# Performance work log

Measured on AMD Instinct MI355X. Metric: run time of the kernel, lower is better.

Reference implementation:

```python
import jax, jax.numpy as jnp
import numpy as np

# Mamba2 config (from AdapterMamba: d_model=1024, n_layer=4, headdim=32; mamba_ssm defaults)
D_MODEL = 1024
N_LAYER = 4
EXPAND = 2
HEADDIM = 32
D_STATE = 128
D_CONV = 4
NGROUPS = 1
D_INNER = EXPAND * D_MODEL            # 2048
NHEADS = D_INNER // HEADDIM           # 64
CONV_DIM = D_INNER + 2 * NGROUPS * D_STATE   # 2304
D_IN_PROJ = 2 * D_INNER + 2 * NGROUPS * D_STATE + NHEADS  # 4416
BATCH, SEQLEN = 4, 2048


def setup_inputs() -> dict:
    key = jax.random.key(0)
    ks = jax.random.split(key, 8)
    x = jax.random.normal(ks[0], (BATCH, SEQLEN, D_MODEL), jnp.float32)
    s_in = 1.0 / np.sqrt(D_MODEL)
    s_out = 1.0 / np.sqrt(D_INNER)
    W_in = jax.random.normal(ks[1], (N_LAYER, D_MODEL, D_IN_PROJ), jnp.float32) * s_in
    conv_w = jax.random.normal(ks[2], (N_LAYER, CONV_DIM, D_CONV), jnp.float32) * 0.5
    conv_b = jnp.zeros((N_LAYER, CONV_DIM), jnp.float32)
    # dt_bias = softplus^{-1}(dt) for dt in [1e-3, 0.1] (mamba dt_init)
    dt = jax.random.uniform(ks[3], (N_LAYER, NHEADS), jnp.float32, 0.001, 0.1)
    dt_bias = jnp.log(jnp.expm1(dt))
    # A in [1, 16] per head (A_init_range)
    A_log = jnp.log(jax.random.uniform(ks[4], (N_LAYER, NHEADS), jnp.float32, 1.0, 16.0))
    D = jnp.ones((N_LAYER, NHEADS), jnp.float32)
    gate_norm_w = jnp.ones((N_LAYER, D_INNER), jnp.float32)
    W_out = jax.random.normal(ks[5], (N_LAYER, D_INNER, D_MODEL), jnp.float32) * s_out
    block_norm_w = jnp.ones((N_LAYER, D_MODEL), jnp.float32)
    final_norm_w = jnp.ones((D_MODEL,), jnp.float32)
    return dict(x=x, W_in=W_in, conv_w=conv_w, conv_b=conv_b, dt_bias=dt_bias,
                A_log=A_log, D=D, gate_norm_w=gate_norm_w, W_out=W_out,
                block_norm_w=block_norm_w, final_norm_w=final_norm_w)


def _rmsnorm(x, w, eps=1e-5):
    return x * jax.lax.rsqrt(jnp.mean(x * x, axis=-1, keepdims=True) + eps) * w


def _mamba2_layer(h, Wi, cw, cb, dtb, Alog, Dh, gw, Wo):
    B, L, _ = h.shape
    zxbcdt = h @ Wi                                        # [B,L,4416]
    z, xBC, dt = jnp.split(zxbcdt, [D_INNER, D_INNER + CONV_DIM], axis=-1)
    # causal depthwise conv1d, width D_CONV, over (x, B, C) channels
    xp = jnp.pad(xBC, ((0, 0), (D_CONV - 1, 0), (0, 0)))
    conv = cb + sum(xp[:, k:k + L, :] * cw[:, k] for k in range(D_CONV))
    xBC = jax.nn.silu(conv)
    xs, Bm, Cm = jnp.split(xBC, [D_INNER, D_INNER + D_STATE], axis=-1)
    xs = xs.reshape(B, L, NHEADS, HEADDIM)                 # [B,L,H,P]
    dt = jax.nn.softplus(dt + dtb)                         # [B,L,H]
    A = -jnp.exp(Alog)                                     # [H]
    dA = jnp.exp(dt * A)                                   # [B,L,H]
    dtx = dt[..., None] * xs                               # [B,L,H,P]

    def step(hs, inp):
        dA_t, dtx_t, B_t, C_t = inp
        # hs: [B,H,P,N]
        hs = hs * dA_t[:, :, None, None] + dtx_t[..., None] * B_t[:, None, None, :]
        y = jnp.einsum('bhpn,bn->bhp', hs, C_t)
        return hs, y

    h0 = jnp.zeros((B, NHEADS, HEADDIM, D_STATE), h.dtype)
    _, ys = jax.lax.scan(step, h0, (dA.swapaxes(0, 1), dtx.swapaxes(0, 1),
                                    Bm.swapaxes(0, 1), Cm.swapaxes(0, 1)))
    y = ys.swapaxes(0, 1) + Dh[None, None, :, None] * xs   # skip term D*x
    y = y.reshape(B, L, D_INNER)
    y = _rmsnorm(y * jax.nn.silu(z), gw)                   # gated RMSNorm (Mamba2)
    return y @ Wo


def reference(x, W_in, conv_w, conv_b, dt_bias, A_log, D, gate_norm_w, W_out,
              block_norm_w, final_norm_w):
    h = x
    for l in range(N_LAYER):
        h = h + _mamba2_layer(_rmsnorm(h, block_norm_w[l]), W_in[l], conv_w[l],
                              conv_b[l], dt_bias[l], A_log[l], D[l],
                              gate_norm_w[l], W_out[l])
    return _rmsnorm(h, final_norm_w)
```

## Files before the change

kernel.cpp:

```cpp
#include <hip/hip_runtime.h>

typedef unsigned short u16;
typedef __bf16 bf16x8 __attribute__((ext_vector_type(8)));
typedef float f32x4 __attribute__((ext_vector_type(4)));
typedef u16 u16x8 __attribute__((ext_vector_type(8)));

#define NLAYER 4
#define DMODEL 1024
#define DINNER 2048
#define NHEADS 64
#define CONVDIM 2304
#define XBCLD 2368
#define DPROJ 4416
#define DPROJP 4608
#define BATCH 4
#define SEQLEN 2048
#define NTOK 8192
#define QC 64
#define NCH (SEQLEN / QC)

__device__ __forceinline__ u16 f2bf(float f) {
  union { float f; unsigned u; } v; v.f = f;
  return (u16)((v.u + 0x7fffu + ((v.u >> 16) & 1u)) >> 16);
}
__device__ __forceinline__ float bf2f(u16 h) {
  union { unsigned u; float f; } v; v.u = (unsigned)h << 16; return v.f;
}

__device__ __forceinline__ float block_sum256(float v) {
  __shared__ float red[4];
  #pragma unroll
  for (int o = 32; o; o >>= 1) v += __shfl_xor(v, o);
  int t = threadIdx.x;
  if ((t & 63) == 0) red[t >> 6] = v;
  __syncthreads();
  return red[0] + red[1] + red[2] + red[3];
}

__device__ __forceinline__ int swz128(int row, int g) { return (row << 7) + (((g ^ (row & 7)) << 3)); }
__device__ __forceinline__ int swz64(int row, int g)  { return (row << 6) + (((g ^ (row & 7)) << 3)); }

#define GLDS16(g, s) __builtin_amdgcn_global_load_lds( \
    (const __attribute__((address_space(1))) void*)(g), \
    (__attribute__((address_space(3))) void*)(s), 16, 0, 0)

#define PH_READ(buf, p)                                                        \
  if ((p) == 0) {                                                              \
    _Pragma("unroll") for (int nf = 0; nf < NF; ++nf)                          \
    _Pragma("unroll") for (int ks = 0; ks < 2; ++ks)                           \
      breg[nf][ks] = readB(buf, nf, ks);                                       \
  }                                                                            \
  _Pragma("unroll") for (int i = 0; i < 2; ++i)                                \
  _Pragma("unroll") for (int ks = 0; ks < 2; ++ks)                             \
    ar[i][ks] = readA(buf, ((p) << 1) + i, ks);

#define PH_TAIL(buf, p)                                                        \
  __builtin_amdgcn_sched_barrier(0);                                           \
  __builtin_amdgcn_s_barrier();                                                \
  asm volatile("s_waitcnt lgkmcnt(0)" ::: "memory");                           \
  __builtin_amdgcn_sched_barrier(0);                                           \
  __builtin_amdgcn_s_setprio(1);                                               \
  _Pragma("unroll") for (int i = 0; i < 2; ++i)                                \
  _Pragma("unroll") for (int nf = 0; nf < NF; ++nf)                            \
  _Pragma("unroll") for (int ks = 0; ks < 2; ++ks)                             \
    acc[((p) << 1) + i][nf] = __builtin_amdgcn_mfma_f32_16x16x32_bf16(         \
        ar[i][ks], breg[nf][ks], acc[((p) << 1) + i][nf], 0, 0, 0);            \
  __builtin_amdgcn_s_setprio(0);                                               \
  __builtin_amdgcn_s_barrier();

template<int NF, int MODE>
__global__ __launch_bounds__(512, 1) void gemm8p_k(
    const u16* __restrict__ A, const u16* __restrict__ Bt,
    float* __restrict__ C, u16* __restrict__ zy, u16* __restrict__ xbc,
    float* __restrict__ dtraw, int K, int nt2) {
  constexpr int NBH = NF / 2;
  __shared__ __align__(16) u16 smem[(2 * (2 + NBH)) * 8192];

  const int tid = threadIdx.x;
  const int w = tid >> 6, l = tid & 63;
  const int wm = w >> 2, wn = w & 3;
  const int l16 = l & 15, kg = l >> 4;
  const int lr = l >> 3, lc = l & 7;
  const int swg = lc ^ lr;

  const int gx = gridDim.x;
  const int nwg = gx * gridDim.y;
  int bid = blockIdx.y * gx + blockIdx.x;
  bid = (bid & 7) * (nwg >> 3) + (bid >> 3);
  const int m0 = (bid / gx) << 8;
  const int n0 = (bid % gx) * (NF << 6);

  f32x4 acc[8][NF] = {};
  bf16x8 breg[NF][2];
  bf16x8 ar[2][2];

  auto stageA = [&](int buf, int h, int kt) {
    const size_t kb = (size_t)(kt << 6) + (swg << 3);
    u16* dst = smem + (((buf << 1) + h) << 13);
    #pragma unroll
    for (int j = 0; j < 2; ++j)
      GLDS16(A + (size_t)(m0 + (h << 7) + (j << 6) + (w << 3) + lr) * K + kb,
             dst + (j << 12) + (w << 9));
  };
  auto stageB = [&](int buf, int h, int kt) {
    const size_t kb = (size_t)(kt << 6) + (swg << 3);
    u16* dst = smem + ((4 + buf * NBH + h) << 13);
    #pragma unroll
    for (int j = 0; j < 2; ++j)
      GLDS16(Bt + (size_t)(n0 + (h << 7) + (j << 6) + (w << 3) + lr) * K + kb,
             dst + (j << 12) + (w << 9));
  };
  auto readA = [&](int buf, int mf, int ks) -> bf16x8 {
    const int r = (mf << 4) + l16;
    return *(const bf16x8*)&smem[(((buf << 1) + wm) << 13) + (r << 6) + ((((ks << 2) + kg) ^ (r & 7)) << 3)];
  };
  auto readB = [&](int buf, int nf, int ks) -> bf16x8 {
    const int row = wn * (NF << 4) + (nf << 4) + l16;
    const int bh = row >> 7, r = row & 127;
    return *(const bf16x8*)&smem[((4 + buf * NBH + bh) << 13) + (r << 6) + ((((ks << 2) + kg) ^ (r & 7)) << 3)];
  };

  stageA(0, 0, 0); stageA(0, 1, 0);
  #pragma unroll
  for (int h = 0; h < NBH; ++h) stageB(0, h, 0);
  #pragma unroll
  for (int h = 0; h < NBH; ++h) stageB(1, h, 1);
  asm volatile("s_waitcnt vmcnt(%0) lgkmcnt(0)" :: "n"(2 * NBH) : "memory");
  __builtin_amdgcn_sched_barrier(0);
  __builtin_amdgcn_s_barrier();

  for (int t = 0; t < nt2; ++t) {
    const int kt0 = t << 1;
    const bool more = (t + 1 < nt2);
    PH_READ(0, 0)
    stageA(1, 0, kt0 + 1);
    PH_TAIL(0, 0)
    PH_READ(0, 1)
    stageA(1, 1, kt0 + 1);
    PH_TAIL(0, 1)
    PH_READ(0, 2)
    if (more) stageB(0, 0, kt0 + 2);
    PH_TAIL(0, 2)
    PH_READ(0, 3)
    if (more && NBH == 2) stageB(0, 1, kt0 + 2);
    if (more) { asm volatile("s_waitcnt vmcnt(%0)" :: "n"(2 * NBH) : "memory"); }
    else      { asm volatile("s_waitcnt vmcnt(0)" ::: "memory"); }
    PH_TAIL(0, 3)
    PH_READ(1, 0)
    if (more) stageA(0, 0, kt0 + 2);
    PH_TAIL(1, 0)
    PH_READ(1, 1)
    if (more) stageA(0, 1, kt0 + 2);
    PH_TAIL(1, 1)
    PH_READ(1, 2)
    if (more) stageB(1, 0, kt0 + 3);
    PH_TAIL(1, 2)
    PH_READ(1, 3)
    if (more && NBH == 2) stageB(1, 1, kt0 + 3);
    if (more) { asm volatile("s_waitcnt vmcnt(%0)" :: "n"(2 * NBH) : "memory"); }
    PH_TAIL(1, 3)
  }

  __syncthreads();
  if (MODE == 1) {
    const int nt = n0 >> 8;
    if (nt == 17) {
      if (wn == 0) {
        #pragma unroll
        for (int mf = 0; mf < 8; ++mf) {
          const int row = m0 + (wm << 7) + (mf << 4) + (kg << 2);
          #pragma unroll
          for (int nf = 0; nf < NF; ++nf) {
            const int dc = (nf << 4) + l16;
            #pragma unroll
            for (int r = 0; r < 4; ++r)
              dtraw[(size_t)(row + r) * 64 + dc] = acc[mf][nf][r];
          }
        }
      }
    } else {
      #pragma unroll
      for (int mf = 0; mf < 8; ++mf) {
        #pragma unroll
        for (int nf = 0; nf < NF; ++nf) {
          const int col = (wn << 6) + (nf << 4) + l16;
          #pragma unroll
          for (int r = 0; r < 4; ++r) {
            const int row = (wm << 7) + (mf << 4) + (kg << 2) + r;
            smem[(row << 8) + (((col >> 3) ^ (row & 7)) << 3) + (col & 7)] = f2bf(acc[mf][nf][r]);
          }
        }
      }
      __syncthreads();
      const int g = l & 31;
      #pragma unroll
      for (int j = 0; j < 16; ++j) {
        const int row = (w << 5) + (j << 1) + (l >> 5);
        u16x8 v = *(const u16x8*)&smem[(row << 8) + ((g ^ (row & 7)) << 3)];
        const size_t grow = (size_t)(m0 + row);
        const int gcol = n0 + (g << 3);
        if (nt < 8) *(u16x8*)&zy[grow * DINNER + gcol] = v;
        else        *(u16x8*)&xbc[grow * XBCLD + (gcol - 2048)] = v;
      }
    }
  } else {
    float* smf = (float*)smem;
    #pragma unroll
    for (int pass = 0; pass < 2; ++pass) {
      if (wm == pass) {
        #pragma unroll
        for (int mf = 0; mf < 8; ++mf) {
          #pragma unroll
          for (int nf = 0; nf < NF; ++nf) {
            const int col = (wn << 5) + (nf << 4) + l16;
            #pragma unroll
            for (int r = 0; r < 4; ++r) {
              const int lrow = (mf << 4) + (kg << 2) + r;
              smf[(lrow << 7) + (((col >> 2) ^ (lrow & 7)) << 2) + (col & 3)] = acc[mf][nf][r];
            }
          }
        }
      }
      __syncthreads();
      const int g = l & 31;
      #pragma unroll
      for (int j = 0; j < 8; ++j) {
        const int lrow = (w << 4) + (j << 1) + (l >> 5);
        f32x4 v = *(const f32x4*)&smf[(lrow << 7) + ((g ^ (lrow & 7)) << 2)];
        float* cp = &C[(size_t)(m0 + (pass << 7) + lrow) * DMODEL + n0 + (g << 2)];
        f32x4 o = *(const f32x4*)cp;
        #pragma unroll
        for (int q = 0; q < 4; ++q) o[q] += v[q];
        *(f32x4*)cp = o;
      }
      __syncthreads();
    }
  }
}

__global__ __launch_bounds__(256) void transpose_cvt_k(
    const float* __restrict__ in, u16* __restrict__ out, int R, int Cin, int Cpad) {
  __shared__ float t[64][65];
  const int c0 = blockIdx.x << 6, r0 = blockIdx.y << 6;
  const int tx = threadIdx.x & 63, ty = threadIdx.x >> 6;
  #pragma unroll
  for (int i = 0; i < 16; ++i) {
    int r = ty + (i << 2);
    int cc = c0 + tx;
    t[r][tx] = (cc < Cin) ? in[(size_t)(r0 + r) * Cin + cc] : 0.f;
  }
  __syncthreads();
  #pragma unroll
  for (int i = 0; i < 16; ++i) {
    int c = ty + (i << 2);
    out[(size_t)(c0 + c) * R + r0 + tx] = f2bf(t[tx][c]);
  }
}

__global__ void copy_k(const float* __restrict__ in, float* __restrict__ out, int n4) {
  int i = blockIdx.x * blockDim.x + threadIdx.x;
  int stride = gridDim.x * blockDim.x;
  for (; i < n4; i += stride)
    *(f32x4*)&out[(size_t)i * 4] = *(const f32x4*)&in[(size_t)i * 4];
}

__global__ __launch_bounds__(256) void rmsnorm_bf16_k(
    const float* __restrict__ in, const float* __restrict__ w, u16* __restrict__ out) {
  const size_t row = blockIdx.x;
  const int t = threadIdx.x;
  f32x4 v = *(const f32x4*)&in[row * DMODEL + t * 4];
  float ss = block_sum256(v[0]*v[0] + v[1]*v[1] + v[2]*v[2] + v[3]*v[3]);
  float sc = rsqrtf(ss * (1.f / DMODEL) + 1e-5f);
  f32x4 wv = *(const f32x4*)&w[t * 4];
  ushort4 o;
  o.x = f2bf(v[0] * sc * wv[0]); o.y = f2bf(v[1] * sc * wv[1]);
  o.z = f2bf(v[2] * sc * wv[2]); o.w = f2bf(v[3] * sc * wv[3]);
  *(ushort4*)&out[row * DMODEL + t * 4] = o;
}

__global__ __launch_bounds__(256) void final_rmsnorm_k(
    const float* __restrict__ in, const float* __restrict__ w, float* __restrict__ out) {
  const size_t row = blockIdx.x;
  const int t = threadIdx.x;
  f32x4 v = *(const f32x4*)&in[row * DMODEL + t * 4];
  float ss = block_sum256(v[0]*v[0] + v[1]*v[1] + v[2]*v[2] + v[3]*v[3]);
  float sc = rsqrtf(ss * (1.f / DMODEL) + 1e-5f);
  f32x4 wv = *(const f32x4*)&w[t * 4];
  f32x4 o;
  #pragma unroll
  for (int j = 0; j < 4; ++j) o[j] = v[j] * sc * wv[j];
  *(f32x4*)&out[row * DMODEL + t * 4] = o;
}

__global__ __launch_bounds__(256) void conv_tr_k(
    const u16* __restrict__ xbc, const float* __restrict__ cw,
    const float* __restrict__ cb, u16* __restrict__ xact, u16* __restrict__ BT) {
  __shared__ __align__(16) u16 xin[67][72];
  __shared__ __align__(16) u16 xtr[64][72];
  const int ch0 = blockIdx.x << 6, tok0 = blockIdx.y << 6;
  const int tid = threadIdx.x;
  const bool bstart = (tok0 & (SEQLEN - 1)) == 0;
  {
    const int rr = tid >> 3, sg = (tid & 7) << 3;
    #pragma unroll
    for (int i = 0; i < 2; ++i) {
      int r = rr + (i << 5);
      if (bstart && r < 3) *(u16x8*)&xin[r][sg] = (u16x8){};
      else *(int4*)&xin[r][sg] = *(const int4*)&xbc[(size_t)(tok0 - 3 + r) * XBCLD + ch0 + sg];
    }
    if (tid < 24) {
      int r = 64 + (tid >> 3), s2 = (tid & 7) << 3;
      *(int4*)&xin[r][s2] = *(const int4*)&xbc[(size_t)(tok0 - 3 + r) * XBCLD + ch0 + s2];
    }
  }
  __syncthreads();
  const int c2 = tid & 31, th = tid >> 5;
  const int c = c2 << 1, tb = th << 3;
  float wv[2][4], bias[2];
  #pragma unroll
  for (int cc = 0; cc < 2; ++cc) {
    bias[cc] = cb[ch0 + c + cc];
    #pragma unroll
    for (int k = 0; k < 4; ++k) wv[cc][k] = cw[(ch0 + c + cc) * 4 + k];
  }
  float m3[2], m2[2], m1[2];
  #pragma unroll
  for (int cc = 0; cc < 2; ++cc) {
    m3[cc] = bf2f(xin[tb][c + cc]);
    m2[cc] = bf2f(xin[tb + 1][c + cc]);
    m1[cc] = bf2f(xin[tb + 2][c + cc]);
  }
  u16 ov[8][2];
  #pragma unroll
  for (int j = 0; j < 8; ++j) {
    #pragma unroll
    for (int cc = 0; cc < 2; ++cc) {
      float xc = bf2f(xin[tb + 3 + j][c + cc]);
      float a = bias[cc] + wv[cc][0]*m3[cc] + wv[cc][1]*m2[cc] + wv[cc][2]*m1[cc] + wv[cc][3]*xc;
      ov[j][cc] = f2bf(a / (1.f + expf(-a)));
      m3[cc] = m2[cc]; m2[cc] = m1[cc]; m1[cc] = xc;
    }
    unsigned pk = (unsigned)ov[j][0] | ((unsigned)ov[j][1] << 16);
    *(unsigned*)&xact[(size_t)(tok0 + tb + j) * CONVDIM + ch0 + c] = pk;
  }
  if (ch0 == 2048 || ch0 == 2112) {
    #pragma unroll
    for (int cc = 0; cc < 2; ++cc) {
      u16x8 v;
      #pragma unroll
      for (int j = 0; j < 8; ++j) v[j] = ov[j][cc];
      *(u16x8*)&xtr[c + cc][tb] = v;
    }
    __syncthreads();
    #pragma unroll
    for (int p = 0; p < 2; ++p) {
      int slot = tid + (p << 8);
      int cc2 = slot >> 3, tseg = slot & 7;
      u16x8 v = *(const u16x8*)&xtr[cc2][tseg << 3];
      *(u16x8*)&BT[(size_t)(ch0 - 2048 + cc2) * NTOK + tok0 + (tseg << 3)] = v;
    }
  }
}

__global__ __launch_bounds__(256, 2) void ssd_local_k(
    const u16* __restrict__ xact, const u16* __restrict__ BT,
    const float* __restrict__ dtraw, const float* __restrict__ dt_bias,
    const float* __restrict__ A_log, const float* __restrict__ Dv,
    u16* __restrict__ ybuf, u16* __restrict__ Sg,
    float* __restrict__ etg, float* __restrict__ decayg) {
  __shared__ __align__(16) u16 Bs[64 * 128];
  __shared__ __align__(16) u16 U[128 * 64];
  __shared__ __align__(16) u16 Xt[32 * 64];
  __shared__ __align__(16) u16 Pl[64 * 64];
  __shared__ float cums[64], dts[64], fac[64];

  const int h = blockIdx.x, ch = blockIdx.y, b = blockIdx.z;
  const int tid = threadIdx.x, w = tid >> 6, l = tid & 63;
  const int l16 = l & 15, kg = l >> 4;
  const size_t tokb = (size_t)b * SEQLEN + (ch << 6);
  const size_t schunk = ((size_t)(b * 64 + h) << 5) + ch;

  const int srow = tid >> 2, sseg = tid & 3;
  int4 creg[4], breg[4], btreg[4];
  #pragma unroll
  for (int i = 0; i < 4; ++i) {
    creg[i] = *(const int4*)&xact[(tokb + srow) * CONVDIM + 2176 + (sseg << 5) + (i << 3)];
    breg[i] = *(const int4*)&xact[(tokb + srow) * CONVDIM + 2048 + (sseg << 5) + (i << 3)];
  }
  const int xtt = tid >> 2, xps = tid & 3;
  int4 xreg = *(const int4*)&xact[(tokb + xtt) * CONVDIM + (h << 5) + (xps << 3)];
  #pragma unroll
  for (int i = 0; i < 4; ++i)
    btreg[i] = *(const int4*)&BT[(size_t)(tid >> 1) * NTOK + tokb + ((((tid & 1) << 2) + i) << 3)];

  #pragma unroll
  for (int i = 0; i < 4; ++i) {
    *(int4*)&U[swz128(srow, (sseg << 2) + i)]  = creg[i];
    *(int4*)&Bs[swz128(srow, (sseg << 2) + i)] = breg[i];
  }
  {
    u16x8 xv = *(const u16x8*)&xreg;
    #pragma unroll
    for (int j = 0; j < 8; ++j) {
      const int pp = (xps << 3) + j;
      Xt[(pp << 6) + ((((xtt >> 3) ^ (pp & 7)) << 3) | (xtt & 7))] = xv[j];
    }
  }

  if (w == 0) {
    float raw = dtraw[(tokb + l) * 64 + h] + dt_bias[h];
    float dtv = raw > 20.f ? raw : log1pf(__expf(raw));
    float cv = -dtv * __expf(A_log[h]);
    #pragma unroll
    for (int d = 1; d < 64; d <<= 1) {
      float o = __shfl_up(cv, d);
      if (l >= d) cv += o;
    }
    float a63 = __shfl(cv, 63);
    cums[l] = cv; dts[l] = dtv; fac[l] = dtv * __expf(a63 - cv);
    etg[(schunk << 6) + l] = __expf(cv);
    if (l == 0) decayg[schunk] = __expf(a63);
  }
  const float Dh = Dv[h];
  __syncthreads();

  f32x4 gacc[4] = {};
  #pragma unroll
  for (int ks = 0; ks < 4; ++ks) {
    bf16x8 ac = *(const bf16x8*)&U[swz128((w << 4) + l16, (ks << 2) + kg)];
    #pragma unroll
    for (int j = 0; j < 4; ++j)
      if (j <= w) {
        bf16x8 bb = *(const bf16x8*)&Bs[swz128((j << 4) + l16, (ks << 2) + kg)];
        gacc[j] = __builtin_amdgcn_mfma_f32_16x16x32_bf16(ac, bb, gacc[j], 0, 0, 0);
      }
  }
  float c_t[4];
  #pragma unroll
  for (int r = 0; r < 4; ++r) c_t[r] = cums[(w << 4) + (kg << 2) + r];
  #pragma unroll
  for (int j = 0; j < 4; ++j) {
    const int s = (j << 4) + l16;
    const float c_s = cums[s], d_s = dts[s];
    #pragma unroll
    for (int r = 0; r < 4; ++r) {
      const int t = (w << 4) + (kg << 2) + r;
      float v = (s <= t) ? gacc[j][r] * __expf(c_t[r] - c_s) * d_s : 0.f;
      Pl[(t << 6) + ((((s >> 3) ^ (t & 7)) << 3) | (s & 7))] = f2bf(v);
    }
  }

  f32x4 y1[2] = {};
  const int nks = (w >> 1) + 1;
  for (int ks = 0; ks < nks; ++ks) {
    bf16x8 ap = *(const bf16x8*)&Pl[swz64((w << 4) + l16, (ks << 2) + kg)];
    #pragma unroll
    for (int pj = 0; pj < 2; ++pj) {
      bf16x8 bx = *(const bf16x8*)&Xt[swz64((pj << 4) + l16, (ks << 2) + kg)];
      y1[pj] = __builtin_amdgcn_mfma_f32_16x16x32_bf16(ap, bx, y1[pj], 0, 0, 0);
    }
  }
  #pragma unroll
  for (int r = 0; r < 4; ++r) {
    const int t = (w << 4) + (kg << 2) + r;
    #pragma unroll
    for (int pj = 0; pj < 2; ++pj) {
      const int p = (pj << 4) + l16;
      float xv = bf2f(Xt[(p << 6) + ((((t >> 3) ^ (p & 7)) << 3) | (t & 7))]);
      ybuf[(tokb + t) * DINNER + (h << 5) + p] = f2bf(y1[pj][r] + Dh * xv);
    }
  }

  __syncthreads();
  #pragma unroll
  for (int i = 0; i < 4; ++i)
    *(int4*)&U[swz64(tid >> 1, ((tid & 1) << 2) + i)] = btreg[i];
  __syncthreads();

  f32x4 sacc[2][2] = {};
  #pragma unroll
  for (int ks = 0; ks < 2; ++ks) {
    float f8[8];
    #pragma unroll
    for (int j = 0; j < 8; ++j) f8[j] = fac[(ks << 5) + (kg << 3) + j];
    #pragma unroll
    for (int pt = 0; pt < 2; ++pt) {
      bf16x8 xr = *(const bf16x8*)&Xt[swz64((pt << 4) + l16, (ks << 2) + kg)];
      bf16x8 xs;
      #pragma unroll
      for (int j = 0; j < 8; ++j) xs[j] = (__bf16)((float)xr[j] * f8[j]);
      #pragma unroll
      for (int nt = 0; nt < 2; ++nt) {
        bf16x8 bb = *(const bf16x8*)&U[swz64(((w << 1) + nt) * 16 + l16, (ks << 2) + kg)];
        sacc[pt][nt] = __builtin_amdgcn_mfma_f32_16x16x32_bf16(xs, bb, sacc[pt][nt], 0, 0, 0);
      }
    }
  }
  u16* sp = Sg + (schunk << 12);
  #pragma unroll
  for (int pt = 0; pt < 2; ++pt)
    #pragma unroll
    for (int nt = 0; nt < 2; ++nt)
      #pragma unroll
      for (int r = 0; r < 4; ++r) {
        const int pr = (pt << 4) + (kg << 2) + r;
        const int n = (w << 5) + (nt << 4) + l16;
        sp[(pr << 7) + n] = f2bf(sacc[pt][nt][r]);
      }
}

__global__ __launch_bounds__(256) void state_scan_k(
    u16* __restrict__ SH, const float* __restrict__ decayg) {
  const int bid = blockIdx.x;
  const size_t base = ((size_t)bid << 17) + ((size_t)threadIdx.x << 4);
  float acc[16] = {};
  u16x8 s0 = *(const u16x8*)&SH[base];
  u16x8 s1 = *(const u16x8*)&SH[base + 8];
  for (int ch = 0; ch < 32; ++ch) {
    const float d = decayg[(bid << 5) + ch];
    u16x8 n0 = {}, n1 = {};
    if (ch + 1 < 32) {
      n0 = *(const u16x8*)&SH[base + ((size_t)(ch + 1) << 12)];
      n1 = *(const u16x8*)&SH[base + ((size_t)(ch + 1) << 12) + 8];
    }
    u16x8 h0, h1;
    #pragma unroll
    for (int j = 0; j < 8; ++j) { h0[j] = f2bf(acc[j]); h1[j] = f2bf(acc[8 + j]); }
    *(u16x8*)&SH[base + ((size_t)ch << 12)] = h0;
    *(u16x8*)&SH[base + ((size_t)ch << 12) + 8] = h1;
    #pragma unroll
    for (int j = 0; j < 8; ++j) {
      acc[j]     = d * acc[j]     + bf2f(s0[j]);
      acc[8 + j] = d * acc[8 + j] + bf2f(s1[j]);
    }
    s0 = n0; s1 = n1;
  }
}

__global__ __launch_bounds__(256) void ssd_cross_k(
    const u16* __restrict__ xact, const u16* __restrict__ Hg,
    const float* __restrict__ etg, u16* __restrict__ ybuf) {
  __shared__ __align__(16) u16 Cs[64 * 128];
  __shared__ __align__(16) u16 Hb[32 * 128];
  __shared__ float etl[64];
  const int h = blockIdx.x, ch = blockIdx.y + 1, b = blockIdx.z;
  const int tid = threadIdx.x, w = tid >> 6, l = tid & 63;
  const int l16 = l & 15, kg = l >> 4;
  const size_t tokb = (size_t)b * SEQLEN + (ch << 6);
  const size_t schunk = ((size_t)(b * 64 + h) << 5) + ch;

  const int srow = tid >> 2, sseg = tid & 3;
  #pragma unroll
  for (int i = 0; i < 4; ++i) {
    int4 v = *(const int4*)&xact[(tokb + srow) * CONVDIM + 2176 + (sseg << 5) + (i << 3)];
    *(int4*)&Cs[swz128(srow, (sseg << 2) + i)] = v;
  }
  const int hp = tid >> 3, hseg = tid & 7;
  #pragma unroll
  for (int i = 0; i < 2; ++i) {
    int4 v = *(const int4*)&Hg[(schunk << 12) + (hp << 7) + (((hseg << 1) + i) << 3)];
    *(int4*)&Hb[swz128(hp, (hseg << 1) + i)] = v;
  }
  if (tid < 64) etl[tid] = etg[(schunk << 6) + tid];
  __syncthreads();

  f32x4 y2[2] = {};
  #pragma unroll
  for (int ks = 0; ks < 4; ++ks) {
    bf16x8 ac = *(const bf16x8*)&Cs[swz128((w << 4) + l16, (ks << 2) + kg)];
    #pragma unroll
    for (int pj = 0; pj < 2; ++pj) {
      bf16x8 bh = *(const bf16x8*)&Hb[swz128((pj << 4) + l16, (ks << 2) + kg)];
      y2[pj] = __builtin_amdgcn_mfma_f32_16x16x32_bf16(ac, bh, y2[pj], 0, 0, 0);
    }
  }
  #pragma unroll
  for (int r = 0; r < 4; ++r) {
    const int t = (w << 4) + (kg << 2) + r;
    const float et = etl[t];
    #pragma unroll
    for (int pj = 0; pj < 2; ++pj) {
      const int p = (pj << 4) + l16;
      const size_t a = (tokb + t) * DINNER + (h << 5) + p;
      ybuf[a] = f2bf(bf2f(ybuf[a]) + et * y2[pj][r]);
    }
  }
}

__global__ __launch_bounds__(256) void gate_rmsnorm_k(
    const u16* __restrict__ y, u16* __restrict__ zy, const float* __restrict__ gw) {
  const size_t row = blockIdx.x;
  const int t = threadIdx.x;
  bf16x8 yv = *(const bf16x8*)&y[row * DINNER + t * 8];
  bf16x8 zv = *(const bf16x8*)&zy[row * DINNER + t * 8];
  float val[8]; float ss = 0.f;
  #pragma unroll
  for (int j = 0; j < 8; ++j) {
    float z = (float)zv[j];
    float v = (float)yv[j] * (z / (1.f + expf(-z)));
    val[j] = v; ss += v * v;
  }
  ss = block_sum256(ss);
  float sc = rsqrtf(ss * (1.f / DINNER) + 1e-5f);
  ushort4 o0, o1;
  o0.x = f2bf(val[0]*sc*gw[t*8+0]); o0.y = f2bf(val[1]*sc*gw[t*8+1]);
  o0.z = f2bf(val[2]*sc*gw[t*8+2]); o0.w = f2bf(val[3]*sc*gw[t*8+3]);
  o1.x = f2bf(val[4]*sc*gw[t*8+4]); o1.y = f2bf(val[5]*sc*gw[t*8+5]);
  o1.z = f2bf(val[6]*sc*gw[t*8+6]); o1.w = f2bf(val[7]*sc*gw[t*8+7]);
  *(ushort4*)&zy[row * DINNER + t * 8] = o0;
  *(ushort4*)&zy[row * DINNER + t * 8 + 4] = o1;
}

extern "C" void kernel_launch(void* const* d_in, const int* in_sizes, int n_in,
                              void* d_out, int out_size, void* d_ws, size_t ws_size,
                              hipStream_t stream) {
  const float* x       = (const float*)d_in[0];
  const float* W_in    = (const float*)d_in[1];
  const float* conv_w  = (const float*)d_in[2];
  const float* conv_b  = (const float*)d_in[3];
  const float* dt_bias = (const float*)d_in[4];
  const float* A_log   = (const float*)d_in[5];
  const float* Dv      = (const float*)d_in[6];
  const float* gate_w  = (const float*)d_in[7];
  const float* W_out   = (const float*)d_in[8];
  const float* block_w = (const float*)d_in[9];
  const float* final_w = (const float*)d_in[10];
  float* out = (float*)d_out;

  char* p = (char*)d_ws;
  auto alloc = [&](size_t bytes) { char* r = p; p += (bytes + 255) & ~(size_t)255; return r; };
  float* hbuf  = (float*)alloc((size_t)NTOK * DMODEL * 4);
  u16*   slabA = (u16*)  alloc((size_t)NTOK * DINNER * 2);
  u16*   slabB = (u16*)  alloc((size_t)NTOK * DINNER * 2);
  u16*   slabC = (u16*)  alloc((size_t)NTOK * CONVDIM * 2);
  u16*   xbc   = (u16*)  alloc((size_t)NTOK * XBCLD * 2);
  float* dtraw = (float*)alloc((size_t)NTOK * NHEADS * 4);
  u16*   BT    = (u16*)  alloc((size_t)128 * NTOK * 2);
  if ((size_t)(p - (char*)d_ws) > ws_size) return;

  u16*   Sg     = (u16*)  alloc((size_t)BATCH * NHEADS * NCH * 4096 * 2);
  float* etg    = (float*)alloc((size_t)BATCH * NHEADS * NCH * 64 * 4);
  float* decayg = (float*)alloc((size_t)BATCH * NHEADS * NCH * 4);
  const bool par = ((size_t)(p - (char*)d_ws) <= ws_size);

  u16* hn   = slabA;
  u16* ybuf = slabA;
  u16* wt   = slabC;
  u16* xact = slabC;

  copy_k<<<2048, 256, 0, stream>>>(x, hbuf, NTOK * DMODEL / 4);

  for (int l = 0; l < NLAYER; ++l) {
    rmsnorm_bf16_k<<<NTOK, 256, 0, stream>>>(hbuf, block_w + l * DMODEL, hn);
    transpose_cvt_k<<<dim3(DPROJP/64, DMODEL/64), 256, 0, stream>>>(
        W_in + (size_t)l * DMODEL * DPROJ, wt, DMODEL, DPROJ, DPROJP);
    gemm8p_k<4, 1><<<dim3(DPROJP/256, NTOK/256), 512, 0, stream>>>(
        hn, wt, nullptr, slabB, xbc, dtraw, DMODEL, DMODEL / 128);
    conv_tr_k<<<dim3(CONVDIM/64, NTOK/64), 256, 0, stream>>>(
        xbc, conv_w + (size_t)l * CONVDIM * 4, conv_b + (size_t)l * CONVDIM, xact, BT);
    if (par) {
      ssd_local_k<<<dim3(NHEADS, NCH, BATCH), 256, 0, stream>>>(
          xact, BT, dtraw, dt_bias + l * NHEADS, A_log + l * NHEADS,
          Dv + l * NHEADS, ybuf, Sg, etg, decayg);
      state_scan_k<<<BATCH * NHEADS, 256, 0, stream>>>(Sg, decayg);
      ssd_cross_k<<<dim3(NHEADS, NCH - 1, BATCH), 256, 0, stream>>>(
          xact, Sg, etg, ybuf);
    }
    gate_rmsnorm_k<<<NTOK, 256, 0, stream>>>(ybuf, slabB, gate_w + (size_t)l * DINNER);
    transpose_cvt_k<<<dim3(DMODEL/64, DINNER/64), 256, 0, stream>>>(
        W_out + (size_t)l * DINNER * DMODEL, wt, DINNER, DMODEL, DMODEL);
    gemm8p_k<2, 0><<<dim3(DMODEL/128, NTOK/256), 512, 0, stream>>>(
        slabB, wt, hbuf, nullptr, nullptr, nullptr, DINNER, DINNER / 128);
  }
  final_rmsnorm_k<<<NTOK, 256, 0, stream>>>(hbuf, final_w, out);
}
```

Before: 1.479 ms.

## Replace 8-wave 256-row GEMM with simpler 128x128 double-buffered 4-wave kernel

Replaces the 512-thread, 256-row-tile GEMM with a hand-phased 8-step pipeline by a 256-thread kernel using 128x128 tiles and plain double buffering. It syncs once per 64-wide k-step and allows two blocks per CU. The goal is higher occupancy and more blocks across the grid to hide latency, instead of the fine-grained intra-block pipeline. The cost is less operand reuse per tile, more global and LDS traffic, and an extra wasted padded column block in the in-projection.

```diff
diff --git a/kernel.cpp b/kernel.cpp
--- a/kernel.cpp
+++ b/kernel.cpp
@@ -44,41 +44,16 @@
     (const __attribute__((address_space(1))) void*)(g), \
     (__attribute__((address_space(3))) void*)(s), 16, 0, 0)
 
-#define PH_READ(buf, p)                                                        \
-  if ((p) == 0) {                                                              \
-    _Pragma("unroll") for (int nf = 0; nf < NF; ++nf)                          \
-    _Pragma("unroll") for (int ks = 0; ks < 2; ++ks)                           \
-      breg[nf][ks] = readB(buf, nf, ks);                                       \
-  }                                                                            \
-  _Pragma("unroll") for (int i = 0; i < 2; ++i)                                \
-  _Pragma("unroll") for (int ks = 0; ks < 2; ++ks)                             \
-    ar[i][ks] = readA(buf, ((p) << 1) + i, ks);
-
-#define PH_TAIL(buf, p)                                                        \
-  __builtin_amdgcn_sched_barrier(0);                                           \
-  __builtin_amdgcn_s_barrier();                                                \
-  asm volatile("s_waitcnt lgkmcnt(0)" ::: "memory");                           \
-  __builtin_amdgcn_sched_barrier(0);                                           \
-  __builtin_amdgcn_s_setprio(1);                                               \
-  _Pragma("unroll") for (int i = 0; i < 2; ++i)                                \
-  _Pragma("unroll") for (int nf = 0; nf < NF; ++nf)                            \
-  _Pragma("unroll") for (int ks = 0; ks < 2; ++ks)                             \
-    acc[((p) << 1) + i][nf] = __builtin_amdgcn_mfma_f32_16x16x32_bf16(         \
-        ar[i][ks], breg[nf][ks], acc[((p) << 1) + i][nf], 0, 0, 0);            \
-  __builtin_amdgcn_s_setprio(0);                                               \
-  __builtin_amdgcn_s_barrier();
-
-template<int NF, int MODE>
-__global__ __launch_bounds__(512, 1) void gemm8p_k(
+template<int MODE>
+__global__ __launch_bounds__(256, 2) void gemm2b_k(
     const u16* __restrict__ A, const u16* __restrict__ Bt,
     float* __restrict__ C, u16* __restrict__ zy, u16* __restrict__ xbc,
-    float* __restrict__ dtraw, int K, int nt2) {
-  constexpr int NBH = NF / 2;
-  __shared__ __align__(16) u16 smem[(2 * (2 + NBH)) * 8192];
+    float* __restrict__ dtraw, int K, int nkt) {
+  __shared__ __align__(16) u16 smem[4 * 8192];
 
   const int tid = threadIdx.x;
   const int w = tid >> 6, l = tid & 63;
-  const int wm = w >> 2, wn = w & 3;
+  const int wm = w >> 1, wn = w & 1;
   const int l16 = l & 15, kg = l >> 4;
   const int lr = l >> 3, lc = l & 7;
   const int swg = lc ^ lr;
@@ -87,90 +62,69 @@
   const int nwg = gx * gridDim.y;
   int bid = blockIdx.y * gx + blockIdx.x;
   bid = (bid & 7) * (nwg >> 3) + (bid >> 3);
-  const int m0 = (bid / gx) << 8;
-  const int n0 = (bid % gx) * (NF << 6);
-
-  f32x4 acc[8][NF] = {};
-  bf16x8 breg[NF][2];
-  bf16x8 ar[2][2];
-
-  auto stageA = [&](int buf, int h, int kt) {
+  const int m0 = (bid / gx) << 7;
+  const int n0 = (bid % gx) << 7;
+
+  f32x4 acc[4][4] = {};
+
+  auto stage = [&](int buf, int kt) {
     const size_t kb = (size_t)(kt << 6) + (swg << 3);
-    u16* dst = smem + (((buf << 1) + h) << 13);
-    #pragma unroll
-    for (int j = 0; j < 2; ++j)
-      GLDS16(A + (size_t)(m0 + (h << 7) + (j << 6) + (w << 3) + lr) * K + kb,
-             dst + (j << 12) + (w << 9));
+    u16* da = smem + (buf << 13);
+    u16* db = smem + ((2 + buf) << 13);
+    #pragma unroll
+    for (int j = 0; j < 4; ++j) {
+      const int r0 = (w << 5) + (j << 3);
+      GLDS16(A + (size_t)(m0 + r0 + lr) * K + kb, da + (r0 << 6));
+      GLDS16(Bt + (size_t)(n0 + r0 + lr) * K + kb, db + (r0 << 6));
+    }
   };
-  auto stageB = [&](int buf, int h, int kt) {
-    const size_t kb = (size_t)(kt << 6) + (swg << 3);
-    u16* dst = smem + ((4 + buf * NBH + h) << 13);
-    #pragma unroll
-    for (int j = 0; j < 2; ++j)
-      GLDS16(Bt + (size_t)(n0 + (h << 7) + (j << 6) + (w << 3) + lr) * K + kb,
-             dst + (j << 12) + (w << 9));
+  auto readA = [&](int cur, int mf, int ks) -> bf16x8 {
+    const int r = (wm << 6) + (mf << 4) + l16;
+    return *(const bf16x8*)&smem[(cur << 13) + (r << 6) + ((((ks << 2) + kg) ^ (r & 7)) << 3)];
   };
-  auto readA = [&](int buf, int mf, int ks) -> bf16x8 {
-    const int r = (mf << 4) + l16;
-    return *(const bf16x8*)&smem[(((buf << 1) + wm) << 13) + (r << 6) + ((((ks << 2) + kg) ^ (r & 7)) << 3)];
+  auto readB = [&](int cur, int nf, int ks) -> bf16x8 {
+    const int r = (wn << 6) + (nf << 4) + l16;
+    return *(const bf16x8*)&smem[((2 + cur) << 13) + (r << 6) + ((((ks << 2) + kg) ^ (r & 7)) << 3)];
   };
-  auto readB = [&](int buf, int nf, int ks) -> bf16x8 {
-    const int row = wn * (NF << 4) + (nf << 4) + l16;
-    const int bh = row >> 7, r = row & 127;
-    return *(const bf16x8*)&smem[((4 + buf * NBH + bh) << 13) + (r << 6) + ((((ks << 2) + kg) ^ (r & 7)) << 3)];
-  };
-
-  stageA(0, 0, 0); stageA(0, 1, 0);
-  #pragma unroll
-  for (int h = 0; h < NBH; ++h) stageB(0, h, 0);
-  #pragma unroll
-  for (int h = 0; h < NBH; ++h) stageB(1, h, 1);
-  asm volatile("s_waitcnt vmcnt(%0) lgkmcnt(0)" :: "n"(2 * NBH) : "memory");
-  __builtin_amdgcn_sched_barrier(0);
-  __builtin_amdgcn_s_barrier();
-
-  for (int t = 0; t < nt2; ++t) {
-    const int kt0 = t << 1;
-    const bool more = (t + 1 < nt2);
-    PH_READ(0, 0)
-    stageA(1, 0, kt0 + 1);
-    PH_TAIL(0, 0)
-    PH_READ(0, 1)
-    stageA(1, 1, kt0 + 1);
-    PH_TAIL(0, 1)
-    PH_READ(0, 2)
-    if (more) stageB(0, 0, kt0 + 2);
-    PH_TAIL(0, 2)
-    PH_READ(0, 3)
-    if (more && NBH == 2) stageB(0, 1, kt0 + 2);
-    if (more) { asm volatile("s_waitcnt vmcnt(%0)" :: "n"(2 * NBH) : "memory"); }
-    else      { asm volatile("s_waitcnt vmcnt(0)" ::: "memory"); }
-    PH_TAIL(0, 3)
-    PH_READ(1, 0)
-    if (more) stageA(0, 0, kt0 + 2);
-    PH_TAIL(1, 0)
-    PH_READ(1, 1)
-    if (more) stageA(0, 1, kt0 + 2);
-    PH_TAIL(1, 1)
-    PH_READ(1, 2)
-    if (more) stageB(1, 0, kt0 + 3);
-    PH_TAIL(1, 2)
-    PH_READ(1, 3)
-    if (more && NBH == 2) stageB(1, 1, kt0 + 3);
-    if (more) { asm volatile("s_waitcnt vmcnt(%0)" :: "n"(2 * NBH) : "memory"); }
-    PH_TAIL(1, 3)
-  }
-
-  __syncthreads();
+
+  stage(0, 0);
+  __syncthreads();
+
+  for (int kt = 0; kt < nkt; ++kt) {
+    const int cur = kt & 1;
+    if (kt + 1 < nkt) stage(cur ^ 1, kt + 1);
+    bf16x8 af[4][2], bq[4][2];
+    #pragma unroll
+    for (int mf = 0; mf < 4; ++mf)
+      #pragma unroll
+      for (int ks = 0; ks < 2; ++ks) af[mf][ks] = readA(cur, mf, ks);
+    #pragma unroll
+    for (int nf = 0; nf < 4; ++nf)
+      #pragma unroll
+      for (int ks = 0; ks < 2; ++ks) bq[nf][ks] = readB(cur, nf, ks);
+    __builtin_amdgcn_s_setprio(1);
+    #pragma unroll
+    for (int mf = 0; mf < 4; ++mf)
+      #pragma unroll
+      for (int nf = 0; nf < 4; ++nf)
+        #pragma unroll
+        for (int ks = 0; ks < 2; ++ks)
+          acc[mf][nf] = __builtin_amdgcn_mfma_f32_16x16x32_bf16(
+              af[mf][ks], bq[nf][ks], acc[mf][nf], 0, 0, 0);
+    __builtin_amdgcn_s_setprio(0);
+    __syncthreads();
+  }
+
   if (MODE == 1) {
-    const int nt = n0 >> 8;
-    if (nt == 17) {
+    const int nt = n0 >> 7;
+    if (nt == 35) return;
+    if (nt == 34) {
       if (wn == 0) {
         #pragma unroll
-        for (int mf = 0; mf < 8; ++mf) {
-          const int row = m0 + (wm << 7) + (mf << 4) + (kg << 2);
+        for (int mf = 0; mf < 4; ++mf) {
+          const int row = m0 + (wm << 6) + (mf << 4) + (kg << 2);
           #pragma unroll
-          for (int nf = 0; nf < NF; ++nf) {
+          for (int nf = 0; nf < 4; ++nf) {
             const int dc = (nf << 4) + l16;
             #pragma unroll
             for (int r = 0; r < 4; ++r)
@@ -178,62 +132,54 @@
           }
         }
       }
-    } else {
-      #pragma unroll
-      for (int mf = 0; mf < 8; ++mf) {
+      return;
+    }
+    #pragma unroll
+    for (int mf = 0; mf < 4; ++mf)
+      #pragma unroll
+      for (int nf = 0; nf < 4; ++nf) {
+        const int col = (wn << 6) + (nf << 4) + l16;
         #pragma unroll
-        for (int nf = 0; nf < NF; ++nf) {
-          const int col = (wn << 6) + (nf << 4) + l16;
-          #pragma unroll
-          for (int r = 0; r < 4; ++r) {
-            const int row = (wm << 7) + (mf << 4) + (kg << 2) + r;
-            smem[(row << 8) + (((col >> 3) ^ (row & 7)) << 3) + (col & 7)] = f2bf(acc[mf][nf][r]);
-          }
+        for (int r = 0; r < 4; ++r) {
+          const int row = (wm << 6) + (mf << 4) + (kg << 2) + r;
+          smem[(row << 7) + (((col >> 3) ^ (row & 7)) << 3) + (col & 7)] = f2bf(acc[mf][nf][r]);
         }
       }
-      __syncthreads();
-      const int g = l & 31;
-      #pragma unroll
-      for (int j = 0; j < 16; ++j) {
-        const int row = (w << 5) + (j << 1) + (l >> 5);
-        u16x8 v = *(const u16x8*)&smem[(row << 8) + ((g ^ (row & 7)) << 3)];
-        const size_t grow = (size_t)(m0 + row);
-        const int gcol = n0 + (g << 3);
-        if (nt < 8) *(u16x8*)&zy[grow * DINNER + gcol] = v;
-        else        *(u16x8*)&xbc[grow * XBCLD + (gcol - 2048)] = v;
-      }
+    __syncthreads();
+    const int g = l & 15;
+    #pragma unroll
+    for (int j = 0; j < 8; ++j) {
+      const int row = (w << 5) + (j << 2) + (l >> 4);
+      u16x8 v = *(const u16x8*)&smem[(row << 7) + ((g ^ (row & 7)) << 3)];
+      const size_t grow = (size_t)(m0 + row);
+      const int gcol = n0 + (g << 3);
+      if (nt < 16) *(u16x8*)&zy[grow * DINNER + gcol] = v;
+      else         *(u16x8*)&xbc[grow * XBCLD + (gcol - 2048)] = v;
     }
   } else {
     float* smf = (float*)smem;
     #pragma unroll
-    for (int pass = 0; pass < 2; ++pass) {
-      if (wm == pass) {
+    for (int mf = 0; mf < 4; ++mf)
+      #pragma unroll
+      for (int nf = 0; nf < 4; ++nf) {
+        const int col = (wn << 6) + (nf << 4) + l16;
         #pragma unroll
-        for (int mf = 0; mf < 8; ++mf) {
-          #pragma unroll
-          for (int nf = 0; nf < NF; ++nf) {
-            const int col = (wn << 5) + (nf << 4) + l16;
-            #pragma unroll
-            for (int r = 0; r < 4; ++r) {
-              const int lrow = (mf << 4) + (kg << 2) + r;
-              smf[(lrow << 7) + (((col >> 2) ^ (lrow & 7)) << 2) + (col & 3)] = acc[mf][nf][r];
-            }
-          }
+        for (int r = 0; r < 4; ++r) {
+          const int row = (wm << 6) + (mf << 4) + (kg << 2) + r;
+          smf[(row << 7) + ((((col >> 2) ^ (row & 7)) << 2) | (col & 3))] = acc[mf][nf][r];
         }
       }
-      __syncthreads();
-      const int g = l & 31;
-      #pragma unroll
-      for (int j = 0; j < 8; ++j) {
-        const int lrow = (w << 4) + (j << 1) + (l >> 5);
-        f32x4 v = *(const f32x4*)&smf[(lrow << 7) + ((g ^ (lrow & 7)) << 2)];
-        float* cp = &C[(size_t)(m0 + (pass << 7) + lrow) * DMODEL + n0 + (g << 2)];
-        f32x4 o = *(const f32x4*)cp;
-        #pragma unroll
-        for (int q = 0; q < 4; ++q) o[q] += v[q];
-        *(f32x4*)cp = o;
-      }
-      __syncthreads();
+    __syncthreads();
+    const int g = l & 31;
+    #pragma unroll
+    for (int j = 0; j < 16; ++j) {
+      const int row = (w << 5) + (j << 1) + (l >> 5);
+      f32x4 v = *(const f32x4*)&smf[(row << 7) + ((g ^ (row & 7)) << 2)];
+      float* cp = &C[(size_t)(m0 + row) * DMODEL + n0 + (g << 2)];
+      f32x4 o = *(const f32x4*)cp;
+      #pragma unroll
+      for (int q = 0; q < 4; ++q) o[q] += v[q];
+      *(f32x4*)cp = o;
     }
   }
 }
@@ -654,8 +600,8 @@
     rmsnorm_bf16_k<<<NTOK, 256, 0, stream>>>(hbuf, block_w + l * DMODEL, hn);
     transpose_cvt_k<<<dim3(DPROJP/64, DMODEL/64), 256, 0, stream>>>(
         W_in + (size_t)l * DMODEL * DPROJ, wt, DMODEL, DPROJ, DPROJP);
-    gemm8p_k<4, 1><<<dim3(DPROJP/256, NTOK/256), 512, 0, stream>>>(
-        hn, wt, nullptr, slabB, xbc, dtraw, DMODEL, DMODEL / 128);
+    gemm2b_k<1><<<dim3(DPROJP/128, NTOK/128), 256, 0, stream>>>(
+        hn, wt, nullptr, slabB, xbc, dtraw, DMODEL, DMODEL / 64);
     conv_tr_k<<<dim3(CONVDIM/64, NTOK/64), 256, 0, stream>>>(
         xbc, conv_w + (size_t)l * CONVDIM * 4, conv_b + (size_t)l * CONVDIM, xact, BT);
     if (par) {
@@ -669,8 +615,8 @@
     gate_rmsnorm_k<<<NTOK, 256, 0, stream>>>(ybuf, slabB, gate_w + (size_t)l * DINNER);
     transpose_cvt_k<<<dim3(DMODEL/64, DINNER/64), 256, 0, stream>>>(
         W_out + (size_t)l * DINNER * DMODEL, wt, DINNER, DMODEL, DMODEL);
-    gemm8p_k<2, 0><<<dim3(DMODEL/128, NTOK/256), 512, 0, stream>>>(
-        slabB, wt, hbuf, nullptr, nullptr, nullptr, DINNER, DINNER / 128);
+    gemm2b_k<0><<<dim3(DMODEL/128, NTOK/128), 256, 0, stream>>>(
+        slabB, wt, hbuf, nullptr, nullptr, nullptr, DINNER, DINNER / 64);
   }
   final_rmsnorm_k<<<NTOK, 256, 0, stream>>>(hbuf, final_w, out);
 }
```

New measurement: 1.455 ms. About the same (-1.6%).
